# Kernel tuning notes

Measured on AMD Instinct MI355X. Metric: run time of the kernel, lower is better.

## Reference

```python
import jax, jax.numpy as jnp
import numpy as np

B, C, L = 4, 512, 4096

def setup_inputs() -> dict:
    key = jax.random.key(0)
    k1, k2, k3, k4 = jax.random.split(key, 4)
    proj_query = jax.random.normal(k1, (B, C, L), dtype=jnp.float32)
    proj_key = jax.random.normal(k2, (B, C, L), dtype=jnp.float32)
    proj_val = jax.random.normal(k3, (B, C, L), dtype=jnp.float32)
    # binary padding mask over key positions, broadcast over query axis
    padding_mask = (jax.random.uniform(k4, (B, 1, L)) < 0.9).astype(jnp.float32)
    return {"proj_query": proj_query, "proj_key": proj_key,
            "proj_val": proj_val, "padding_mask": padding_mask}

def reference(proj_query, proj_key, proj_val, padding_mask):
    c = proj_query.shape[1]
    # energy[b,i,j] = sum_c Q[b,c,i] * K[b,c,j]  -> (B, L1, L2)
    energy = jnp.einsum('bci,bcj->bij', proj_query, proj_key)
    attention = energy / jnp.sqrt(jnp.asarray(c, dtype=energy.dtype))
    attention = attention + jnp.log(padding_mask + 1e-6)
    attention = jax.nn.softmax(attention, axis=-1)
    attention = attention * padding_mask
    attention = attention.transpose(0, 2, 1)  # (B, L2, L1)
    out = jnp.einsum('bcj,bji->bci', proj_val, attention)  # (B, C, L1)
    return out, attention
```

## Files before the change

kernel.cpp:

```cpp
#include <hip/hip_runtime.h>

#define B_ 4
#define C_ 512
#define L_ 4096

typedef __attribute__((ext_vector_type(8))) short bf16x8;
typedef __attribute__((ext_vector_type(4))) float f32x4;

#define MFMA16(a, b, c) __builtin_amdgcn_mfma_f32_16x16x32_bf16(a, b, c, 0, 0, 0)

static __device__ __forceinline__ unsigned short f2bf_rne(float f) {
  unsigned u = __float_as_uint(f);
  u += 0x7FFFu + ((u >> 16) & 1u);
  return (unsigned short)(u >> 16);
}
static __device__ __forceinline__ unsigned pack_rne(float a, float b) {
  return (unsigned)f2bf_rne(a) | ((unsigned)f2bf_rne(b) << 16);
}
static __device__ __forceinline__ float bflo2f(unsigned w) {
  return __uint_as_float(w << 16);
}
static __device__ __forceinline__ float bfhi2f(unsigned w) {
  return __uint_as_float(w & 0xFFFF0000u);
}

static __device__ __forceinline__ void g2lds16(const unsigned short* g,
                                               unsigned short* l) {
  __builtin_amdgcn_global_load_lds(
      (const __attribute__((address_space(1))) unsigned int*)g,
      (__attribute__((address_space(3))) unsigned int*)l, 16, 0, 0);
}

#define BAR_() __builtin_amdgcn_s_barrier()
#define LGKM0_() asm volatile("s_waitcnt lgkmcnt(0)" ::: "memory")
#define VMW_(N) asm volatile("s_waitcnt vmcnt(" #N ")" ::: "memory")

__global__ __launch_bounds__(256) void prep_k(
    const float* __restrict__ Q, const float* __restrict__ K,
    const float* __restrict__ V, const float* __restrict__ mask,
    unsigned short* __restrict__ Qt, unsigned short* __restrict__ Kt,
    unsigned short* __restrict__ Vb, float* __restrict__ rowsum) {
  int zb = blockIdx.z;
  int t = threadIdx.x;
  __shared__ float tile[64][65];
  if (zb < 8) {
    int b = zb >> 1;
    const float* src = ((zb & 1) ? K : Q) + (size_t)b * C_ * L_;
    unsigned short* dst = ((zb & 1) ? Kt : Qt) + (size_t)b * L_ * C_;
    int i0 = blockIdx.x * 64, c0 = blockIdx.y * 64;
    int cr = t >> 2, ig = (t & 3) * 16;
    const float* s = src + (size_t)(c0 + cr) * L_ + i0 + ig;
#pragma unroll
    for (int q = 0; q < 4; ++q) {
      float4 v = *(const float4*)(s + 4 * q);
      tile[cr][ig + 4 * q + 0] = v.x;
      tile[cr][ig + 4 * q + 1] = v.y;
      tile[cr][ig + 4 * q + 2] = v.z;
      tile[cr][ig + 4 * q + 3] = v.w;
    }
    __syncthreads();
    int ir = t >> 2, cg = (t & 3) * 16;
    unsigned wds[8];
#pragma unroll
    for (int k = 0; k < 8; ++k)
      wds[k] = pack_rne(tile[cg + 2 * k][ir], tile[cg + 2 * k + 1][ir]);
    unsigned short* d = dst + (size_t)(i0 + ir) * C_ + c0 + cg;
    uint4 o0, o1;
    o0.x = wds[0]; o0.y = wds[1]; o0.z = wds[2]; o0.w = wds[3];
    o1.x = wds[4]; o1.y = wds[5]; o1.z = wds[6]; o1.w = wds[7];
    *(uint4*)d = o0;
    *(uint4*)(d + 8) = o1;
  } else {
    int b = zb - 8;
    int flat = blockIdx.x + (blockIdx.y << 6);
    if (b == 0 && flat == 0) {
      float4 z4 = {0.f, 0.f, 0.f, 0.f};
#pragma unroll
      for (int q = 0; q < 16; ++q)
        *(float4*)(rowsum + (q * 256 + t) * 4) = z4;
    }
    size_t base = (size_t)b * C_ * L_ + (size_t)flat * 4096 + (size_t)t * 16;
    int j = (int)(base & (L_ - 1));
    const float* vp = V + base;
    const float* mp = mask + (size_t)b * L_ + j;
#pragma unroll
    for (int g = 0; g < 2; ++g) {
      float4 v0 = *(const float4*)(vp + g * 8);
      float4 v1 = *(const float4*)(vp + g * 8 + 4);
      float4 m0 = *(const float4*)(mp + g * 8);
      float4 m1 = *(const float4*)(mp + g * 8 + 4);
      uint4 o;
      o.x = pack_rne(v0.x * m0.x, v0.y * m0.y);
      o.y = pack_rne(v0.z * m0.z, v0.w * m0.w);
      o.z = pack_rne(v1.x * m1.x, v1.y * m1.y);
      o.w = pack_rne(v1.z * m1.z, v1.w * m1.w);
      *(uint4*)(Vb + base + g * 8) = o;
    }
  }
}

__device__ __forceinline__ void gemm_8phase(
    const unsigned short* __restrict__ Ab,
    const unsigned short* __restrict__ Bb, int lda, int ldb, int Kdim,
    unsigned short* sA, unsigned short* sB, f32x4 (&acc)[8][4]) {
  const int t = threadIdx.x;
  const int lane = t & 63;
  const int quad = lane >> 4;
  const int l15 = lane & 15;
  const int w = t >> 6;
  const int wm = (w & 1) * 128;
  const int wn = (w >> 1) * 64;
  const int et = (t * 8) ^ (((t >> 5) & 1) << 4);
  const int srw = et >> 5;
  const int scl = et & 31;
  const int nt = Kdim >> 6;

  auto stage = [&](int nom, int hh) {
    int st = nom < nt ? nom : nt - 1;
    int db = nom & 1;
    int h = hh & 1;
    const unsigned short* g;
    unsigned short* l;
    if (hh < 2) {
      g = Bb + (size_t)(h * 128 + srw) * ldb + st * 64 + scl;
      l = sB + db * 16384 + h * 4096 + t * 8;
    } else {
      g = Ab + (size_t)(h * 128 + srw) * lda + st * 64 + scl;
      l = sA + db * 16384 + h * 4096 + t * 8;
    }
    g2lds16(g, l);
    g2lds16(g + 32, l + 8192);
  };
  auto rd = [&](const unsigned short* s, int db, int kc, int row) -> bf16x8 {
    int e = db * 16384 + kc * 8192 + row * 32 + quad * 8;
    e ^= ((e >> 8) & 1) << 4;
    return *(const bf16x8*)(s + e);
  };

  bf16x8 aF[4][2], b0[2][2], b1[2][2];
  auto rdA4 = [&](int db, int mbase) {
#pragma unroll
    for (int m = 0; m < 4; ++m)
#pragma unroll
      for (int kc = 0; kc < 2; ++kc)
        aF[m][kc] = rd(sA, db, kc, wm + (mbase + m) * 16 + l15);
  };
  auto rdB2 = [&](bf16x8 (&bf)[2][2], int db, int nbase) {
#pragma unroll
    for (int n = 0; n < 2; ++n)
#pragma unroll
      for (int kc = 0; kc < 2; ++kc)
        bf[n][kc] = rd(sB, db, kc, wn + (nbase + n) * 16 + l15);
  };
  auto mfma8 = [&](bf16x8 (&bf)[2][2], int mo, int no) {
    __builtin_amdgcn_s_setprio(1);
#pragma unroll
    for (int m = 0; m < 4; ++m)
#pragma unroll
      for (int n = 0; n < 2; ++n) {
        acc[mo + m][no + n] = MFMA16(aF[m][0], bf[n][0], acc[mo + m][no + n]);
        acc[mo + m][no + n] = MFMA16(aF[m][1], bf[n][1], acc[mo + m][no + n]);
      }
    __builtin_amdgcn_s_setprio(0);
  };

  stage(0, 0); stage(0, 1); stage(0, 2); stage(0, 3);
  asm volatile("s_waitcnt vmcnt(4)" ::: "memory");
  stage(1, 0); stage(1, 1); stage(1, 2);
  asm volatile("s_waitcnt vmcnt(6)" ::: "memory");
  BAR_();

  const int ni = nt >> 1;
  for (int i = 0; i < ni; ++i) {
    const int X = 2 * i;
    rdA4(0, 0); rdB2(b0, 0, 0); rdB2(b1, 0, 2);
    stage(X + 1, 3);
    BAR_(); LGKM0_();
    mfma8(b0, 0, 0);
    BAR_();
    stage(X + 2, 0);
    BAR_();
    mfma8(b1, 0, 2);
    BAR_();
    rdA4(0, 4);
    stage(X + 2, 1);
    BAR_(); LGKM0_();
    mfma8(b0, 4, 0);
    BAR_();
    stage(X + 2, 2);
    VMW_(6); BAR_();
    mfma8(b1, 4, 2);
    BAR_(); __builtin_amdgcn_sched_barrier(0);
    rdA4(1, 0); rdB2(b0, 1, 0); rdB2(b1, 1, 2);
    stage(X + 2, 3);
    BAR_(); LGKM0_();
    mfma8(b0, 0, 0);
    BAR_();
    stage(X + 3, 0);
    BAR_();
    mfma8(b1, 0, 2);
    BAR_();
    rdA4(1, 4);
    stage(X + 3, 1);
    BAR_(); LGKM0_();
    mfma8(b0, 4, 0);
    BAR_();
    stage(X + 3, 2);
    VMW_(6); BAR_();
    mfma8(b1, 4, 2);
    BAR_(); __builtin_amdgcn_sched_barrier(0);
  }
  asm volatile("s_waitcnt vmcnt(0)" ::: "memory");
}

__global__ __launch_bounds__(512, 2) void gemm1_8p_k(
    const unsigned short* __restrict__ Qt, const unsigned short* __restrict__ Kt,
    const float* __restrict__ mask, unsigned short* __restrict__ t0,
    unsigned short* __restrict__ t1, unsigned short* __restrict__ t2,
    unsigned short* __restrict__ t3, float* __restrict__ rowsum) {
  __shared__ unsigned short sA[32768];
  __shared__ unsigned short sB[32768];
  int flat = blockIdx.x + (blockIdx.y << 4) + (blockIdx.z << 8);
  int swz = (flat & 7) * 128 + (flat >> 3);
  int bx = swz & 15, by = (swz >> 4) & 15, b = swz >> 8;
  unsigned short* tbb = (b == 0) ? t0 : (b == 1) ? t1 : (b == 2) ? t2 : t3;
  int i0 = by * 256, j0 = bx * 256;
  f32x4 acc[8][4] = {};
  gemm_8phase(Qt + (size_t)b * L_ * C_ + (size_t)i0 * C_,
              Kt + (size_t)b * L_ * C_ + (size_t)j0 * C_, C_, C_, C_, sA, sB,
              acc);
  int t = threadIdx.x;
  int lane = t & 63;
  int quad = lane >> 4;
  int l15 = lane & 15;
  int w = t >> 6;
  int wm = (w & 1) * 128;
  int wn = (w >> 1) * 64;
  const float scale = 0.04419417382415922f;
  float lm[4], mv[4];
#pragma unroll
  for (int n = 0; n < 4; ++n) {
    int j = j0 + wn + n * 16 + l15;
    float m = mask[(size_t)b * L_ + j];
    mv[n] = m;
    lm[n] = __logf(m + 1e-6f);
  }
  float rs[8][4];
#pragma unroll
  for (int m = 0; m < 8; ++m)
#pragma unroll
    for (int r = 0; r < 4; ++r) rs[m][r] = 0.f;
#pragma unroll
  for (int m = 0; m < 8; ++m) {
    int irow = i0 + wm + m * 16 + quad * 4;
#pragma unroll
    for (int r = 0; r < 4; ++r) {
      size_t ro = (size_t)(irow + r) * L_;
#pragma unroll
      for (int n = 0; n < 4; ++n) {
        float x = fminf(acc[m][n][r] * scale + lm[n], 60.f);
        float tv = __expf(x);
        rs[m][r] += tv;
        tbb[ro + j0 + wn + n * 16 + l15] = f2bf_rne(tv * mv[n]);
      }
    }
  }
#pragma unroll
  for (int mm = 1; mm < 16; mm <<= 1)
#pragma unroll
    for (int m = 0; m < 8; ++m)
#pragma unroll
      for (int r = 0; r < 4; ++r) rs[m][r] += __shfl_xor(rs[m][r], mm, 64);
  if (l15 == 0) {
    float* rb = rowsum + (size_t)b * L_ + i0 + wm;
#pragma unroll
    for (int m = 0; m < 8; ++m)
#pragma unroll
      for (int r = 0; r < 4; ++r)
        atomicAdd(&rb[m * 16 + quad * 4 + r], rs[m][r]);
  }
}

__global__ __launch_bounds__(512, 2) void gemm2_8p_k(
    const unsigned short* __restrict__ Vb, const unsigned short* __restrict__ t0,
    const unsigned short* __restrict__ t1, const unsigned short* __restrict__ t2,
    const unsigned short* __restrict__ t3, const float* __restrict__ rowsum,
    float* __restrict__ out, float* __restrict__ out2) {
  __shared__ unsigned short sA[32768];
  __shared__ unsigned short sB[32768];
  int flat = blockIdx.x + (blockIdx.y << 4) + (blockIdx.z << 5);
  int swz = (flat & 7) * 32 + (flat >> 3);
  int ix = swz & 15, cy = (swz >> 4) & 1, z = swz >> 5;
  int b = z & 3, ks = z >> 2;
  const unsigned short* tbb =
      (b == 0) ? t0 : (b == 1) ? t1 : (b == 2) ? t2 : t3;
  int i0 = ix * 256, c0 = cy * 256;
  f32x4 acc[8][4] = {};
  gemm_8phase(Vb + (size_t)b * C_ * L_ + (size_t)c0 * L_ + ks * (L_ / 2),
              tbb + (size_t)i0 * L_ + ks * (L_ / 2), L_, L_, L_ / 2, sA, sB,
              acc);
  int t = threadIdx.x;
  int lane = t & 63;
  int quad = lane >> 4;
  int l15 = lane & 15;
  int w = t >> 6;
  int wm = (w & 1) * 128;
  int wn = (w >> 1) * 64;
  float invv[4];
#pragma unroll
  for (int n = 0; n < 4; ++n)
    invv[n] = 1.0f / rowsum[(size_t)b * L_ + i0 + wn + n * 16 + l15];
  float* ob = (ks ? out2 : out) + (size_t)b * C_ * L_;
#pragma unroll
  for (int m = 0; m < 8; ++m) {
    int crow = c0 + wm + m * 16 + quad * 4;
#pragma unroll
    for (int r = 0; r < 4; ++r) {
      size_t ro = (size_t)(crow + r) * L_;
#pragma unroll
      for (int n = 0; n < 4; ++n)
        ob[ro + i0 + wn + n * 16 + l15] = acc[m][n][r] * invv[n];
    }
  }
}

__global__ __launch_bounds__(256) void finalize_all_k(
    const unsigned short* __restrict__ tb, const float* __restrict__ rowsum,
    float* __restrict__ attn, float* __restrict__ out,
    const float* __restrict__ out2) {
  int b = blockIdx.z;
  int t = threadIdx.x;
  if (out2 != nullptr) {
    int flat = blockIdx.x + (blockIdx.y << 6) + (blockIdx.z << 12);
    if (flat < 8192) {
      size_t idx = (size_t)flat * 1024 + (size_t)t * 4;
      float4 a = *(const float4*)(out + idx);
      float4 c = *(const float4*)(out2 + idx);
      a.x += c.x; a.y += c.y; a.z += c.z; a.w += c.w;
      *(float4*)(out + idx) = a;
    }
  }
  const unsigned short* src = tb + (size_t)b * L_ * L_;
  const float* rs = rowsum + (size_t)b * L_;
  float* dst = attn + (size_t)b * L_ * L_;
  int jt = blockIdx.x, it = blockIdx.y;
  __shared__ float tileT[64][65];
  int r = t >> 2, cg = (t & 3) * 16;
  int i = it * 64 + r;
  float inv = 1.0f / rs[i];
  const unsigned short* sp = src + (size_t)i * L_ + jt * 64 + cg;
  uint4 u0 = *(const uint4*)sp;
  uint4 u1 = *(const uint4*)(sp + 8);
  const unsigned* w0 = (const unsigned*)&u0;
  const unsigned* w1 = (const unsigned*)&u1;
#pragma unroll
  for (int k = 0; k < 4; ++k) {
    tileT[cg + 2 * k + 0][r] = bflo2f(w0[k]) * inv;
    tileT[cg + 2 * k + 1][r] = bfhi2f(w0[k]) * inv;
    tileT[cg + 8 + 2 * k + 0][r] = bflo2f(w1[k]) * inv;
    tileT[cg + 8 + 2 * k + 1][r] = bfhi2f(w1[k]) * inv;
  }
  __syncthreads();
  float* dp = dst + (size_t)(jt * 64 + r) * L_ + it * 64 + cg;
#pragma unroll
  for (int q = 0; q < 4; ++q) {
    float4 o;
    o.x = tileT[r][cg + 4 * q + 0];
    o.y = tileT[r][cg + 4 * q + 1];
    o.z = tileT[r][cg + 4 * q + 2];
    o.w = tileT[r][cg + 4 * q + 3];
    *(float4*)(dp + 4 * q) = o;
  }
}

__device__ __forceinline__ void gemm_mainloop64(
    const unsigned short* Ab, const unsigned short* Bb, int lda, int ldb,
    int Kdim, unsigned short* sA, unsigned short* sB, f32x4 acc[4][4]) {
  int t = threadIdx.x;
  const unsigned short* pA[4];
  const unsigned short* pB[4];
#pragma unroll
  for (int c = 0; c < 4; ++c) {
    int e = t * 8 + c * 2048;
    int kc = e >> 12;
    int rem = e & 4095;
    int row = rem >> 5;
    int col = rem & 31;
    int off = kc * 32 + col;
    pA[c] = Ab + (size_t)row * lda + off;
    pB[c] = Bb + (size_t)row * ldb + off;
  }
  int lane = t & 63;
  int quad = lane >> 4;
  int l15 = lane & 15;
  int w = t >> 6;
  int wm = (w & 1) * 64;
  int wn = (w >> 1) * 64;
  for (int kk = 0; kk < Kdim; kk += 64) {
    __syncthreads();
#pragma unroll
    for (int c = 0; c < 4; ++c) g2lds16(pA[c] + kk, sA + t * 8 + c * 2048);
#pragma unroll
    for (int c = 0; c < 4; ++c) g2lds16(pB[c] + kk, sB + t * 8 + c * 2048);
    __syncthreads();
#pragma unroll
    for (int kc = 0; kc < 2; ++kc) {
      bf16x8 aF[4], bF[4];
#pragma unroll
      for (int ti = 0; ti < 4; ++ti)
        aF[ti] = *(const bf16x8*)(sA + kc * 4096 +
                                  (wm + ti * 16 + l15) * 32 + quad * 8);
#pragma unroll
      for (int tj = 0; tj < 4; ++tj)
        bF[tj] = *(const bf16x8*)(sB + kc * 4096 +
                                  (wn + tj * 16 + l15) * 32 + quad * 8);
#pragma unroll
      for (int ti = 0; ti < 4; ++ti)
#pragma unroll
        for (int tj = 0; tj < 4; ++tj)
          acc[ti][tj] = MFMA16(aF[ti], bF[tj], acc[ti][tj]);
    }
  }
}

__global__ __launch_bounds__(256) void gemm1_bf_k(
    const unsigned short* __restrict__ Qt, const unsigned short* __restrict__ Kt,
    const float* __restrict__ mask, unsigned short* __restrict__ t0,
    unsigned short* __restrict__ t1, unsigned short* __restrict__ t2,
    unsigned short* __restrict__ t3, float* __restrict__ rowsum) {
  int b = blockIdx.z;
  unsigned short* tbb = (b == 0) ? t0 : (b == 1) ? t1 : (b == 2) ? t2 : t3;
  int i0 = blockIdx.y * 128;
  int j0 = blockIdx.x * 128;
  __shared__ unsigned short sA[8192];
  __shared__ unsigned short sB[8192];
  f32x4 acc[4][4] = {};
  gemm_mainloop64(Qt + (size_t)b * L_ * C_ + (size_t)i0 * C_,
                  Kt + (size_t)b * L_ * C_ + (size_t)j0 * C_, C_, C_, C_, sA,
                  sB, acc);
  int t = threadIdx.x;
  int lane = t & 63;
  int quad = lane >> 4;
  int l15 = lane & 15;
  int w = t >> 6;
  int wm = (w & 1) * 64;
  int wn = (w >> 1) * 64;
  const float scale = 0.04419417382415922f;
  float lm[4], mv[4];
#pragma unroll
  for (int tj = 0; tj < 4; ++tj) {
    int j = j0 + wn + tj * 16 + l15;
    float m = mask[(size_t)b * L_ + j];
    mv[tj] = m;
    lm[tj] = __logf(m + 1e-6f);
  }
  float rs[16];
#pragma unroll
  for (int q = 0; q < 16; ++q) rs[q] = 0.f;
#pragma unroll
  for (int ti = 0; ti < 4; ++ti) {
    int irow = i0 + wm + ti * 16 + quad * 4;
#pragma unroll
    for (int r = 0; r < 4; ++r) {
      size_t ro = (size_t)(irow + r) * L_;
#pragma unroll
      for (int tj = 0; tj < 4; ++tj) {
        float x = fminf(acc[ti][tj][r] * scale + lm[tj], 60.f);
        float tv = __expf(x);
        rs[ti * 4 + r] += tv;
        tbb[ro + j0 + wn + tj * 16 + l15] = f2bf_rne(tv * mv[tj]);
      }
    }
  }
#pragma unroll
  for (int m = 1; m < 16; m <<= 1)
#pragma unroll
    for (int q = 0; q < 16; ++q) rs[q] += __shfl_xor(rs[q], m, 64);
  if (l15 == 0) {
    float* rb = rowsum + (size_t)b * L_ + i0 + wm;
#pragma unroll
    for (int ti = 0; ti < 4; ++ti)
#pragma unroll
      for (int r = 0; r < 4; ++r)
        atomicAdd(&rb[ti * 16 + quad * 4 + r], rs[ti * 4 + r]);
  }
}

__global__ __launch_bounds__(256) void gemm2_bf_k(
    const unsigned short* __restrict__ Vb, const unsigned short* __restrict__ t0,
    const unsigned short* __restrict__ t1, const unsigned short* __restrict__ t2,
    const unsigned short* __restrict__ t3, const float* __restrict__ rowsum,
    float* __restrict__ out) {
  int z = blockIdx.z;
  int b = z & 3;
  int ks = z >> 2;
  const unsigned short* tbb =
      (b == 0) ? t0 : (b == 1) ? t1 : (b == 2) ? t2 : t3;
  int c0 = blockIdx.y * 128;
  int i0 = blockIdx.x * 128;
  __shared__ unsigned short sA[8192];
  __shared__ unsigned short sB[8192];
  f32x4 acc[4][4] = {};
  gemm_mainloop64(Vb + (size_t)b * C_ * L_ + (size_t)c0 * L_ + ks * (L_ / 2),
                  tbb + (size_t)i0 * L_ + ks * (L_ / 2), L_, L_, L_ / 2, sA, sB,
                  acc);
  int t = threadIdx.x;
  int lane = t & 63;
  int quad = lane >> 4;
  int l15 = lane & 15;
  int w = t >> 6;
  int wm = (w & 1) * 64;
  int wn = (w >> 1) * 64;
  float invv[4];
#pragma unroll
  for (int tj = 0; tj < 4; ++tj)
    invv[tj] = 1.0f / rowsum[(size_t)b * L_ + i0 + wn + tj * 16 + l15];
  float* ob = out + (size_t)b * C_ * L_;
#pragma unroll
  for (int ti = 0; ti < 4; ++ti) {
    int crow = c0 + wm + ti * 16 + quad * 4;
#pragma unroll
    for (int r = 0; r < 4; ++r) {
      size_t ro = (size_t)(crow + r) * L_;
#pragma unroll
      for (int tj = 0; tj < 4; ++tj)
        atomicAdd(&ob[ro + i0 + wn + tj * 16 + l15],
                  acc[ti][tj][r] * invv[tj]);
    }
  }
}

extern "C" void kernel_launch(void* const* d_in, const int* in_sizes, int n_in,
                              void* d_out, int out_size, void* d_ws,
                              size_t ws_size, hipStream_t stream) {
  const float* Q = (const float*)d_in[0];
  const float* K = (const float*)d_in[1];
  const float* V = (const float*)d_in[2];
  const float* mask = (const float*)d_in[3];

  float* out = (float*)d_out;
  float* attn = out + (size_t)B_ * C_ * L_;

  const size_t NQ = (size_t)B_ * L_ * C_;
  const size_t SLOT = (size_t)L_ * L_;
  unsigned short* Qt = (unsigned short*)d_ws;
  unsigned short* Kt = Qt + NQ;
  unsigned short* Vb = Kt + NQ;
  float* rowsum = (float*)(Vb + NQ);
  unsigned short* wtail = (unsigned short*)(rowsum + (size_t)B_ * L_);

  const size_t need1 =
      NQ * 2 * 3 + (size_t)B_ * L_ * 4 + (size_t)B_ * SLOT * 2 + NQ * 4;

  prep_k<<<dim3(64, 8, 12), 256, 0, stream>>>(Q, K, V, mask, Qt, Kt, Vb,
                                              rowsum);

  if (ws_size >= need1) {
    unsigned short* tb = wtail;
    float* out2 = (float*)(tb + (size_t)B_ * SLOT);
    gemm1_8p_k<<<dim3(16, 16, B_), 512, 0, stream>>>(
        Qt, Kt, mask, tb, tb + SLOT, tb + 2 * SLOT, tb + 3 * SLOT, rowsum);
    gemm2_8p_k<<<dim3(16, 2, B_ * 2), 512, 0, stream>>>(
        Vb, tb, tb + SLOT, tb + 2 * SLOT, tb + 3 * SLOT, rowsum, out, out2);
    finalize_all_k<<<dim3(64, 64, B_), 256, 0, stream>>>(tb, rowsum, attn, out,
                                                         out2);
  } else {
    unsigned short* tb0 = (unsigned short*)(attn + 2 * SLOT);
    unsigned short* tb1 = (unsigned short*)(attn + 3 * SLOT);
    unsigned short* tb2 = (unsigned short*)(attn + 3 * SLOT + SLOT / 2);
    unsigned short* tb3 = wtail;
    hipMemsetAsync(out, 0, (size_t)B_ * C_ * L_ * sizeof(float), stream);
    gemm1_bf_k<<<dim3(L_ / 128, L_ / 128, B_), 256, 0, stream>>>(
        Qt, Kt, mask, tb0, tb1, tb2, tb3, rowsum);
    gemm2_bf_k<<<dim3(L_ / 128, C_ / 128, B_ * 2), 256, 0, stream>>>(
        Vb, tb0, tb1, tb2, tb3, rowsum, out);
    finalize_all_k<<<dim3(64, 64, 1), 256, 0, stream>>>(tb0, rowsum, attn,
                                                        nullptr, nullptr);
    finalize_all_k<<<dim3(64, 64, 1), 256, 0, stream>>>(tb1, rowsum + L_,
                                                        attn + SLOT, nullptr,
                                                        nullptr);
    finalize_all_k<<<dim3(64, 64, 1), 256, 0, stream>>>(tb2, rowsum + 2 * L_,
                                                        attn + 2 * SLOT,
                                                        nullptr, nullptr);
    finalize_all_k<<<dim3(64, 64, 1), 256, 0, stream>>>(tb3, rowsum + 3 * L_,
                                                        attn + 3 * SLOT,
                                                        nullptr, nullptr);
  }
}
```

Before: 653.1 us.

## Fuse attention finalize into second GEMM launch and split out combine

Replaces the 256x256 8-phase second GEMM with a 128x128 tile GEMM that shares one launch with the attention transpose/normalize blocks. The blocks that write the attention matrix can then overlap with the GEMM blocks instead of running in a later launch. The out+out2 reduction moves into its own small kernel. In exchange the GEMM tiles are smaller and less efficient, with more global traffic per flop and a simpler single-buffered mainloop.

```diff
diff --git a/kernel.cpp b/kernel.cpp
--- a/kernel.cpp
+++ b/kernel.cpp
@@ -281,68 +281,155 @@
   }
 }
 
-__global__ __launch_bounds__(512, 2) void gemm2_8p_k(
-    const unsigned short* __restrict__ Vb, const unsigned short* __restrict__ t0,
-    const unsigned short* __restrict__ t1, const unsigned short* __restrict__ t2,
-    const unsigned short* __restrict__ t3, const float* __restrict__ rowsum,
-    float* __restrict__ out, float* __restrict__ out2) {
-  __shared__ unsigned short sA[32768];
-  __shared__ unsigned short sB[32768];
-  int flat = blockIdx.x + (blockIdx.y << 4) + (blockIdx.z << 5);
-  int swz = (flat & 7) * 32 + (flat >> 3);
-  int ix = swz & 15, cy = (swz >> 4) & 1, z = swz >> 5;
-  int b = z & 3, ks = z >> 2;
-  const unsigned short* tbb =
-      (b == 0) ? t0 : (b == 1) ? t1 : (b == 2) ? t2 : t3;
-  int i0 = ix * 256, c0 = cy * 256;
-  f32x4 acc[8][4] = {};
-  gemm_8phase(Vb + (size_t)b * C_ * L_ + (size_t)c0 * L_ + ks * (L_ / 2),
-              tbb + (size_t)i0 * L_ + ks * (L_ / 2), L_, L_, L_ / 2, sA, sB,
-              acc);
+__device__ __forceinline__ void gemm_mainloop64(
+    const unsigned short* Ab, const unsigned short* Bb, int lda, int ldb,
+    int Kdim, unsigned short* sA, unsigned short* sB, f32x4 acc[4][4]) {
   int t = threadIdx.x;
+  const unsigned short* pA[4];
+  const unsigned short* pB[4];
+#pragma unroll
+  for (int c = 0; c < 4; ++c) {
+    int e = t * 8 + c * 2048;
+    int kc = e >> 12;
+    int rem = e & 4095;
+    int row = rem >> 5;
+    int col = rem & 31;
+    int off = kc * 32 + col;
+    pA[c] = Ab + (size_t)row * lda + off;
+    pB[c] = Bb + (size_t)row * ldb + off;
+  }
   int lane = t & 63;
   int quad = lane >> 4;
   int l15 = lane & 15;
   int w = t >> 6;
-  int wm = (w & 1) * 128;
+  int wm = (w & 1) * 64;
   int wn = (w >> 1) * 64;
-  float invv[4];
-#pragma unroll
-  for (int n = 0; n < 4; ++n)
-    invv[n] = 1.0f / rowsum[(size_t)b * L_ + i0 + wn + n * 16 + l15];
-  float* ob = (ks ? out2 : out) + (size_t)b * C_ * L_;
-#pragma unroll
-  for (int m = 0; m < 8; ++m) {
-    int crow = c0 + wm + m * 16 + quad * 4;
-#pragma unroll
-    for (int r = 0; r < 4; ++r) {
-      size_t ro = (size_t)(crow + r) * L_;
-#pragma unroll
-      for (int n = 0; n < 4; ++n)
-        ob[ro + i0 + wn + n * 16 + l15] = acc[m][n][r] * invv[n];
-    }
-  }
-}
-
-__global__ __launch_bounds__(256) void finalize_all_k(
+  for (int kk = 0; kk < Kdim; kk += 64) {
+    __syncthreads();
+#pragma unroll
+    for (int c = 0; c < 4; ++c) g2lds16(pA[c] + kk, sA + t * 8 + c * 2048);
+#pragma unroll
+    for (int c = 0; c < 4; ++c) g2lds16(pB[c] + kk, sB + t * 8 + c * 2048);
+    __syncthreads();
+#pragma unroll
+    for (int kc = 0; kc < 2; ++kc) {
+      bf16x8 aF[4], bF[4];
+#pragma unroll
+      for (int ti = 0; ti < 4; ++ti)
+        aF[ti] = *(const bf16x8*)(sA + kc * 4096 +
+                                  (wm + ti * 16 + l15) * 32 + quad * 8);
+#pragma unroll
+      for (int tj = 0; tj < 4; ++tj)
+        bF[tj] = *(const bf16x8*)(sB + kc * 4096 +
+                                  (wn + tj * 16 + l15) * 32 + quad * 8);
+#pragma unroll
+      for (int ti = 0; ti < 4; ++ti)
+#pragma unroll
+        for (int tj = 0; tj < 4; ++tj)
+          acc[ti][tj] = MFMA16(aF[ti], bF[tj], acc[ti][tj]);
+    }
+  }
+}
+
+__global__ __launch_bounds__(256) void gemm2_fin_k(
+    const unsigned short* __restrict__ Vb, const unsigned short* __restrict__ t0,
+    const unsigned short* __restrict__ t1, const unsigned short* __restrict__ t2,
+    const unsigned short* __restrict__ t3, const float* __restrict__ rowsum,
+    float* __restrict__ out, float* __restrict__ out2,
+    float* __restrict__ attn) {
+  __shared__ __align__(16) unsigned char smem[32768];
+  int fb = blockIdx.x;
+  int t = threadIdx.x;
+  if (fb < 1024) {
+    unsigned short* sA = (unsigned short*)smem;
+    unsigned short* sB = (unsigned short*)(smem + 16384);
+    int ix = fb & 31, cy = (fb >> 5) & 3, z = fb >> 7;
+    int b = z & 3, ks = z >> 2;
+    const unsigned short* tbb =
+        (b == 0) ? t0 : (b == 1) ? t1 : (b == 2) ? t2 : t3;
+    int i0 = ix * 128, c0 = cy * 128;
+    f32x4 acc[4][4] = {};
+    gemm_mainloop64(Vb + (size_t)b * C_ * L_ + (size_t)c0 * L_ + ks * (L_ / 2),
+                    tbb + (size_t)i0 * L_ + ks * (L_ / 2), L_, L_, L_ / 2, sA,
+                    sB, acc);
+    int lane = t & 63;
+    int quad = lane >> 4;
+    int l15 = lane & 15;
+    int w = t >> 6;
+    int wm = (w & 1) * 64;
+    int wn = (w >> 1) * 64;
+    float invv[4];
+#pragma unroll
+    for (int tj = 0; tj < 4; ++tj)
+      invv[tj] = 1.0f / rowsum[(size_t)b * L_ + i0 + wn + tj * 16 + l15];
+    float* ob = (ks ? out2 : out) + (size_t)b * C_ * L_;
+#pragma unroll
+    for (int ti = 0; ti < 4; ++ti) {
+      int crow = c0 + wm + ti * 16 + quad * 4;
+#pragma unroll
+      for (int r = 0; r < 4; ++r) {
+        size_t ro = (size_t)(crow + r) * L_;
+#pragma unroll
+        for (int tj = 0; tj < 4; ++tj)
+          ob[ro + i0 + wn + tj * 16 + l15] = acc[ti][tj][r] * invv[tj];
+      }
+    }
+  } else {
+    float(*tileT)[65] = (float(*)[65])smem;
+    int g = fb - 1024;
+    int jt = g & 63, it = (g >> 6) & 63, b = g >> 12;
+    const unsigned short* src = t0 + (size_t)b * L_ * L_;
+    const float* rs = rowsum + (size_t)b * L_;
+    float* dst = attn + (size_t)b * L_ * L_;
+    int r = t >> 2, cg = (t & 3) * 16;
+    int i = it * 64 + r;
+    float inv = 1.0f / rs[i];
+    const unsigned short* sp = src + (size_t)i * L_ + jt * 64 + cg;
+    uint4 u0 = *(const uint4*)sp;
+    uint4 u1 = *(const uint4*)(sp + 8);
+    const unsigned* w0 = (const unsigned*)&u0;
+    const unsigned* w1 = (const unsigned*)&u1;
+#pragma unroll
+    for (int k = 0; k < 4; ++k) {
+      tileT[cg + 2 * k + 0][r] = bflo2f(w0[k]) * inv;
+      tileT[cg + 2 * k + 1][r] = bfhi2f(w0[k]) * inv;
+      tileT[cg + 8 + 2 * k + 0][r] = bflo2f(w1[k]) * inv;
+      tileT[cg + 8 + 2 * k + 1][r] = bfhi2f(w1[k]) * inv;
+    }
+    __syncthreads();
+    float* dp = dst + (size_t)(jt * 64 + r) * L_ + it * 64 + cg;
+#pragma unroll
+    for (int q = 0; q < 4; ++q) {
+      float4 o;
+      o.x = tileT[r][cg + 4 * q + 0];
+      o.y = tileT[r][cg + 4 * q + 1];
+      o.z = tileT[r][cg + 4 * q + 2];
+      o.w = tileT[r][cg + 4 * q + 3];
+      *(float4*)(dp + 4 * q) = o;
+    }
+  }
+}
+
+__global__ __launch_bounds__(256) void combine_out_k(
+    float* __restrict__ out, const float* __restrict__ out2) {
+  size_t idx = ((size_t)blockIdx.x * 256 + threadIdx.x) * 8;
+  float4 a0 = *(const float4*)(out + idx);
+  float4 a1 = *(const float4*)(out + idx + 4);
+  float4 b0 = *(const float4*)(out2 + idx);
+  float4 b1 = *(const float4*)(out2 + idx + 4);
+  a0.x += b0.x; a0.y += b0.y; a0.z += b0.z; a0.w += b0.w;
+  a1.x += b1.x; a1.y += b1.y; a1.z += b1.z; a1.w += b1.w;
+  *(float4*)(out + idx) = a0;
+  *(float4*)(out + idx + 4) = a1;
+}
+
+__global__ __launch_bounds__(256) void finalize_one_k(
     const unsigned short* __restrict__ tb, const float* __restrict__ rowsum,
-    float* __restrict__ attn, float* __restrict__ out,
-    const float* __restrict__ out2) {
-  int b = blockIdx.z;
+    float* __restrict__ attn) {
   int t = threadIdx.x;
-  if (out2 != nullptr) {
-    int flat = blockIdx.x + (blockIdx.y << 6) + (blockIdx.z << 12);
-    if (flat < 8192) {
-      size_t idx = (size_t)flat * 1024 + (size_t)t * 4;
-      float4 a = *(const float4*)(out + idx);
-      float4 c = *(const float4*)(out2 + idx);
-      a.x += c.x; a.y += c.y; a.z += c.z; a.w += c.w;
-      *(float4*)(out + idx) = a;
-    }
-  }
-  const unsigned short* src = tb + (size_t)b * L_ * L_;
-  const float* rs = rowsum + (size_t)b * L_;
-  float* dst = attn + (size_t)b * L_ * L_;
+  const unsigned short* src = tb;
+  const float* rs = rowsum;
+  float* dst = attn;
   int jt = blockIdx.x, it = blockIdx.y;
   __shared__ float tileT[64][65];
   int r = t >> 2, cg = (t & 3) * 16;
@@ -370,56 +457,6 @@
     o.z = tileT[r][cg + 4 * q + 2];
     o.w = tileT[r][cg + 4 * q + 3];
     *(float4*)(dp + 4 * q) = o;
-  }
-}
-
-__device__ __forceinline__ void gemm_mainloop64(
-    const unsigned short* Ab, const unsigned short* Bb, int lda, int ldb,
-    int Kdim, unsigned short* sA, unsigned short* sB, f32x4 acc[4][4]) {
-  int t = threadIdx.x;
-  const unsigned short* pA[4];
-  const unsigned short* pB[4];
-#pragma unroll
-  for (int c = 0; c < 4; ++c) {
-    int e = t * 8 + c * 2048;
-    int kc = e >> 12;
-    int rem = e & 4095;
-    int row = rem >> 5;
-    int col = rem & 31;
-    int off = kc * 32 + col;
-    pA[c] = Ab + (size_t)row * lda + off;
-    pB[c] = Bb + (size_t)row * ldb + off;
-  }
-  int lane = t & 63;
-  int quad = lane >> 4;
-  int l15 = lane & 15;
-  int w = t >> 6;
-  int wm = (w & 1) * 64;
-  int wn = (w >> 1) * 64;
-  for (int kk = 0; kk < Kdim; kk += 64) {
-    __syncthreads();
-#pragma unroll
-    for (int c = 0; c < 4; ++c) g2lds16(pA[c] + kk, sA + t * 8 + c * 2048);
-#pragma unroll
-    for (int c = 0; c < 4; ++c) g2lds16(pB[c] + kk, sB + t * 8 + c * 2048);
-    __syncthreads();
-#pragma unroll
-    for (int kc = 0; kc < 2; ++kc) {
-      bf16x8 aF[4], bF[4];
-#pragma unroll
-      for (int ti = 0; ti < 4; ++ti)
-        aF[ti] = *(const bf16x8*)(sA + kc * 4096 +
-                                  (wm + ti * 16 + l15) * 32 + quad * 8);
-#pragma unroll
-      for (int tj = 0; tj < 4; ++tj)
-        bF[tj] = *(const bf16x8*)(sB + kc * 4096 +
-                                  (wn + tj * 16 + l15) * 32 + quad * 8);
-#pragma unroll
-      for (int ti = 0; ti < 4; ++ti)
-#pragma unroll
-        for (int tj = 0; tj < 4; ++tj)
-          acc[ti][tj] = MFMA16(aF[ti], bF[tj], acc[ti][tj]);
-    }
   }
 }
 
@@ -560,10 +597,10 @@
     float* out2 = (float*)(tb + (size_t)B_ * SLOT);
     gemm1_8p_k<<<dim3(16, 16, B_), 512, 0, stream>>>(
         Qt, Kt, mask, tb, tb + SLOT, tb + 2 * SLOT, tb + 3 * SLOT, rowsum);
-    gemm2_8p_k<<<dim3(16, 2, B_ * 2), 512, 0, stream>>>(
-        Vb, tb, tb + SLOT, tb + 2 * SLOT, tb + 3 * SLOT, rowsum, out, out2);
-    finalize_all_k<<<dim3(64, 64, B_), 256, 0, stream>>>(tb, rowsum, attn, out,
-                                                         out2);
+    gemm2_fin_k<<<dim3(1024 + 16384), 256, 0, stream>>>(
+        Vb, tb, tb + SLOT, tb + 2 * SLOT, tb + 3 * SLOT, rowsum, out, out2,
+        attn);
+    combine_out_k<<<dim3((B_ * C_ * L_) / 2048), 256, 0, stream>>>(out, out2);
   } else {
     unsigned short* tb0 = (unsigned short*)(attn + 2 * SLOT);
     unsigned short* tb1 = (unsigned short*)(attn + 3 * SLOT);
@@ -574,16 +611,12 @@
         Qt, Kt, mask, tb0, tb1, tb2, tb3, rowsum);
     gemm2_bf_k<<<dim3(L_ / 128, C_ / 128, B_ * 2), 256, 0, stream>>>(
         Vb, tb0, tb1, tb2, tb3, rowsum, out);
-    finalize_all_k<<<dim3(64, 64, 1), 256, 0, stream>>>(tb0, rowsum, attn,
-                                                        nullptr, nullptr);
-    finalize_all_k<<<dim3(64, 64, 1), 256, 0, stream>>>(tb1, rowsum + L_,
-                                                        attn + SLOT, nullptr,
-                                                        nullptr);
-    finalize_all_k<<<dim3(64, 64, 1), 256, 0, stream>>>(tb2, rowsum + 2 * L_,
-                                                        attn + 2 * SLOT,
-                                                        nullptr, nullptr);
-    finalize_all_k<<<dim3(64, 64, 1), 256, 0, stream>>>(tb3, rowsum + 3 * L_,
-                                                        attn + 3 * SLOT,
-                                                        nullptr, nullptr);
-  }
-}
+    finalize_one_k<<<dim3(64, 64, 1), 256, 0, stream>>>(tb0, rowsum, attn);
+    finalize_one_k<<<dim3(64, 64, 1), 256, 0, stream>>>(tb1, rowsum + L_,
+                                                        attn + SLOT);
+    finalize_one_k<<<dim3(64, 64, 1), 256, 0, stream>>>(tb2, rowsum + 2 * L_,
+                                                        attn + 2 * SLOT);
+    finalize_one_k<<<dim3(64, 64, 1), 256, 0, stream>>>(tb3, rowsum + 3 * L_,
+                                                        attn + 3 * SLOT);
+  }
+}
```

Measured after the change: 678.3 us. +3.8%, slower.
